# Optimization experiments

Measured on AMD Instinct MI355X. Metric: run time of the kernel, lower is better.

## Reference

```python
import jax, jax.numpy as jnp
import numpy as np

B, L, D_MODEL = 2, 2048, 1024
D_INNER, D_STATE, D_CONV, DT_RANK = 2048, 16, 4, 64  # expand=2, dt_rank=ceil(1024/16)


def setup_inputs() -> dict:
    key = jax.random.key(0)
    ks = jax.random.split(key, 12)
    s = lambda k, shape, sc=0.02: jax.random.normal(k, shape, dtype=jnp.float32) * sc
    return {
        "x": jax.random.normal(ks[0], (B, L, D_MODEL), dtype=jnp.float32),
        "norm_w": jnp.ones((D_MODEL,), jnp.float32),
        "norm_b": jnp.zeros((D_MODEL,), jnp.float32),
        "in_proj_w": s(ks[1], (2 * D_INNER, D_MODEL)),
        "conv_w": s(ks[2], (D_INNER, 1, D_CONV), 0.1),
        "conv_b": s(ks[3], (D_INNER,), 0.1),
        "x_proj_w": s(ks[4], (DT_RANK + 2 * D_STATE, D_INNER)),
        "dt_proj_w": s(ks[5], (D_INNER, DT_RANK), 0.1),
        "dt_proj_b": s(ks[6], (D_INNER,), 0.5),
        "A_log": jnp.log(jnp.broadcast_to(jnp.arange(1, D_STATE + 1, dtype=jnp.float32), (D_INNER, D_STATE))),
        "D": jnp.ones((D_INNER,), jnp.float32),
        "out_proj_w": s(ks[7], (D_MODEL, D_INNER)),
    }


def _layernorm(x, w, b, eps=1e-5):
    mu = jnp.mean(x, axis=-1, keepdims=True)
    var = jnp.var(x, axis=-1, keepdims=True)
    return (x - mu) * jax.lax.rsqrt(var + eps) * w + b


def _mamba_forward(x, norm_w, norm_b, in_proj_w, conv_w, conv_b, x_proj_w,
                   dt_proj_w, dt_proj_b, A_log, D, out_proj_w):
    residual = x
    xn = _layernorm(x, norm_w, norm_b)
    # in_proj -> split into x-branch and gate z
    xz = jnp.einsum('bld,ed->ble', xn, in_proj_w)  # [B,L,2*D_INNER]
    xc, z = jnp.split(xz, 2, axis=-1)
    # causal depthwise conv1d over time
    xt = jnp.transpose(xc, (0, 2, 1))  # [B,C,L]
    xt = jnp.pad(xt, ((0, 0), (0, 0), (D_CONV - 1, 0)))
    xt = jax.lax.conv_general_dilated(
        xt, conv_w, window_strides=(1,), padding=[(0, 0)],
        feature_group_count=D_INNER,
        dimension_numbers=('NCH', 'OIH', 'NCH')) + conv_b[None, :, None]
    u = jax.nn.silu(jnp.transpose(xt, (0, 2, 1)))  # [B,L,D_INNER]
    # input-dependent dt, B, C
    x_dbl = jnp.einsum('bld,ed->ble', u, x_proj_w)
    dt, Bm, Cm = jnp.split(x_dbl, [DT_RANK, DT_RANK + D_STATE], axis=-1)
    dt = jax.nn.softplus(jnp.einsum('blr,dr->bld', dt, dt_proj_w) + dt_proj_b)  # [B,L,D_INNER]
    A = -jnp.exp(A_log)  # [D_INNER, D_STATE]

    def step(h, inp):
        dt_t, B_t, C_t, u_t = inp  # [B,Di],[B,Ds],[B,Ds],[B,Di]
        dA = jnp.exp(dt_t[..., None] * A)                       # [B,Di,Ds]
        h = dA * h + (dt_t * u_t)[..., None] * B_t[:, None, :]  # [B,Di,Ds]
        y_t = jnp.einsum('bds,bs->bd', h, C_t)
        return h, y_t

    xs = (jnp.transpose(dt, (1, 0, 2)), jnp.transpose(Bm, (1, 0, 2)),
          jnp.transpose(Cm, (1, 0, 2)), jnp.transpose(u, (1, 0, 2)))
    h0 = jnp.zeros((B, D_INNER, D_STATE), dtype=x.dtype)
    _, ys = jax.lax.scan(step, h0, xs)
    y = jnp.transpose(ys, (1, 0, 2)) + u * D  # [B,L,D_INNER]
    y = y * jax.nn.silu(z)
    out = jnp.einsum('ble,de->bld', y, out_proj_w)
    # dropout in eval mode = identity
    return residual + out


def reference(x, norm_w, norm_b, in_proj_w, conv_w, conv_b, x_proj_w,
              dt_proj_w, dt_proj_b, A_log, D, out_proj_w):
    return _mamba_forward(x, norm_w, norm_b, in_proj_w, conv_w, conv_b, x_proj_w,
                          dt_proj_w, dt_proj_b, A_log, D, out_proj_w)
```

## Files before the change

kernel.cpp:

```cpp
#include <hip/hip_runtime.h>
#include <hip/hip_bf16.h>
#include <math.h>

#define BB 2
#define LL 2048
#define DMODEL 1024
#define DINNER 2048
#define DSTATE 16
#define DTRANK 64
#define NROWS (BB * LL)
#define NC 32
#define CK 64

typedef __bf16 bf16x8 __attribute__((ext_vector_type(8)));
typedef float  f32x4  __attribute__((ext_vector_type(4)));
typedef __attribute__((address_space(3))) void       as3_void;
typedef const __attribute__((address_space(1))) void as1_cvoid;

__device__ __forceinline__ ushort f2bf(float x) {
    __hip_bfloat16 h = __float2bfloat16(x);
    return *(ushort*)&h;
}

__global__ __launch_bounds__(256) void ln_kernel(const float* __restrict__ x,
                                                 const float* __restrict__ w,
                                                 const float* __restrict__ b,
                                                 __hip_bfloat16* __restrict__ xn) {
    int row = blockIdx.x;
    const float* xr = x + (size_t)row * DMODEL;
    float4 v = reinterpret_cast<const float4*>(xr)[threadIdx.x];
    float s  = v.x + v.y + v.z + v.w;
    float ss = v.x * v.x + v.y * v.y + v.z * v.z + v.w * v.w;
    for (int off = 32; off > 0; off >>= 1) {
        s  += __shfl_down(s, off);
        ss += __shfl_down(ss, off);
    }
    __shared__ float red0[4], red1[4];
    __shared__ float mu_s, rstd_s;
    int lane = threadIdx.x & 63, wv = threadIdx.x >> 6;
    if (lane == 0) { red0[wv] = s; red1[wv] = ss; }
    __syncthreads();
    if (threadIdx.x == 0) {
        float S = red0[0] + red0[1] + red0[2] + red0[3];
        float SS = red1[0] + red1[1] + red1[2] + red1[3];
        float mu = S * (1.0f / DMODEL);
        float var = SS * (1.0f / DMODEL) - mu * mu;
        mu_s = mu;
        rstd_s = rsqrtf(var + 1e-5f);
    }
    __syncthreads();
    float mu = mu_s, rstd = rstd_s;
    float4 wv4 = reinterpret_cast<const float4*>(w)[threadIdx.x];
    float4 bv4 = reinterpret_cast<const float4*>(b)[threadIdx.x];
    ushort4 o;
    o.x = f2bf((v.x - mu) * rstd * wv4.x + bv4.x);
    o.y = f2bf((v.y - mu) * rstd * wv4.y + bv4.y);
    o.z = f2bf((v.z - mu) * rstd * wv4.z + bv4.z);
    o.w = f2bf((v.w - mu) * rstd * wv4.w + bv4.w);
    *reinterpret_cast<ushort4*>((ushort*)xn + (size_t)row * DMODEL + threadIdx.x * 4) = o;
}

__global__ __launch_bounds__(256) void cvt_kernel(const float* __restrict__ in,
                                                  __hip_bfloat16* __restrict__ o) {
    int i = (blockIdx.x * 256 + threadIdx.x) * 4;
    float4 v = *reinterpret_cast<const float4*>(in + i);
    ushort4 p;
    p.x = f2bf(v.x); p.y = f2bf(v.y); p.z = f2bf(v.z); p.w = f2bf(v.w);
    *reinterpret_cast<ushort4*>((ushort*)o + i) = p;
}

template <int EPI>
__global__ __launch_bounds__(256) void gemm_bf16(
    const __hip_bfloat16* __restrict__ A, int lda,
    const __hip_bfloat16* __restrict__ W, int ldw,
    float* __restrict__ C, float* __restrict__ C2, int nsplit, int ldc,
    int K, const float* __restrict__ R) {
    __shared__ ushort As[128][32];
    __shared__ ushort Bs[128][32];
    int tid = threadIdx.x;
    int w = tid >> 6, lane = tid & 63;
    int m0 = blockIdx.y * 128, n0 = blockIdx.x * 128;
    int wr = w >> 1, wc = w & 1;

    int srow = (w << 4) + (lane >> 2);
    int skoff = (lane & 3) << 3;
    const ushort* gA = (const ushort*)A + (size_t)(m0 + srow) * lda + skoff;
    const ushort* gB = (const ushort*)W + (size_t)(n0 + srow) * ldw + skoff;
    char* ldsA0 = (char*)&As[0][0] + w * 1024;
    char* ldsB0 = (char*)&Bs[0][0] + w * 1024;

    f32x4 acc[4][4] = {};
    int frow = (lane & 15);
    int fk   = (lane >> 4) << 3;

    for (int k0 = 0; k0 < K; k0 += 32) {
        __syncthreads();
        __builtin_amdgcn_global_load_lds((as1_cvoid*)(gA + k0),                 (as3_void*)(ldsA0),        16, 0, 0);
        __builtin_amdgcn_global_load_lds((as1_cvoid*)(gA + (size_t)64 * lda + k0), (as3_void*)(ldsA0 + 4096), 16, 0, 0);
        __builtin_amdgcn_global_load_lds((as1_cvoid*)(gB + k0),                 (as3_void*)(ldsB0),        16, 0, 0);
        __builtin_amdgcn_global_load_lds((as1_cvoid*)(gB + (size_t)64 * ldw + k0), (as3_void*)(ldsB0 + 4096), 16, 0, 0);
        __syncthreads();

        bf16x8 af[4], bfr[4];
#pragma unroll
        for (int mi = 0; mi < 4; mi++)
            af[mi] = *(const bf16x8*)&As[wr * 64 + mi * 16 + frow][fk];
#pragma unroll
        for (int ni = 0; ni < 4; ni++)
            bfr[ni] = *(const bf16x8*)&Bs[wc * 64 + ni * 16 + frow][fk];
#pragma unroll
        for (int mi = 0; mi < 4; mi++)
#pragma unroll
            for (int ni = 0; ni < 4; ni++)
                acc[mi][ni] = __builtin_amdgcn_mfma_f32_16x16x32_bf16(
                    af[mi], bfr[ni], acc[mi][ni], 0, 0, 0);
    }

    int crow = (lane >> 4) << 2;
    int ccol = lane & 15;
    float* Cb = C;
    int nbase = n0;
    if (EPI == 0 && n0 >= nsplit) { Cb = C2; nbase = n0 - nsplit; }
#pragma unroll
    for (int mi = 0; mi < 4; mi++) {
#pragma unroll
        for (int ni = 0; ni < 4; ni++) {
#pragma unroll
            for (int r = 0; r < 4; r++) {
                int m = m0 + wr * 64 + mi * 16 + crow + r;
                int n = nbase + wc * 64 + ni * 16 + ccol;
                float v = acc[mi][ni][r];
                if (EPI == 2) v += R[(size_t)m * ldc + n];
                Cb[(size_t)m * ldc + n] = v;
            }
        }
    }
}

template <int EPI>
__global__ __launch_bounds__(256) void gemm_kernel(
    const float* __restrict__ A, int lda,
    const float* __restrict__ W, int ldw,
    float* __restrict__ C, int ldc,
    int N, int K,
    const float* __restrict__ bias) {
    __shared__ float As[16][64];
    __shared__ float Ws[16][64];
    int m0 = blockIdx.y * 64;
    int n0 = blockIdx.x * 64;
    int tid = threadIdx.x;
    int tm = tid >> 4, tn = tid & 15;
    int lr = tid >> 2;
    int lk = (tid & 3) << 2;

    float acc[4][4] = {};

    for (int k0 = 0; k0 < K; k0 += 16) {
        float4 av = *reinterpret_cast<const float4*>(A + (size_t)(m0 + lr) * lda + k0 + lk);
        float4 wvv;
        int wn = n0 + lr;
        if (wn < N)
            wvv = *reinterpret_cast<const float4*>(W + (size_t)wn * ldw + k0 + lk);
        else
            wvv = make_float4(0.f, 0.f, 0.f, 0.f);
        __syncthreads();
        As[lk + 0][lr] = av.x; As[lk + 1][lr] = av.y;
        As[lk + 2][lr] = av.z; As[lk + 3][lr] = av.w;
        Ws[lk + 0][lr] = wvv.x; Ws[lk + 1][lr] = wvv.y;
        Ws[lk + 2][lr] = wvv.z; Ws[lk + 3][lr] = wvv.w;
        __syncthreads();
#pragma unroll
        for (int k = 0; k < 16; k++) {
            float4 a = *reinterpret_cast<const float4*>(&As[k][tm << 2]);
            float4 bv = *reinterpret_cast<const float4*>(&Ws[k][tn << 2]);
            float ar[4] = {a.x, a.y, a.z, a.w};
            float br[4] = {bv.x, bv.y, bv.z, bv.w};
#pragma unroll
            for (int i = 0; i < 4; i++)
#pragma unroll
                for (int j = 0; j < 4; j++)
                    acc[i][j] = fmaf(ar[i], br[j], acc[i][j]);
        }
    }
#pragma unroll
    for (int i = 0; i < 4; i++) {
        int m = m0 + (tm << 2) + i;
#pragma unroll
        for (int j = 0; j < 4; j++) {
            int n = n0 + (tn << 2) + j;
            if (n < N) {
                float v = acc[i][j];
                if (EPI == 1) {
                    v += bias[n];
                    v = (v > 20.f) ? v : log1pf(__expf(v));
                }
                C[(size_t)m * ldc + n] = v;
            }
        }
    }
}

__global__ __launch_bounds__(256) void conv_silu_kernel(
    const float* __restrict__ xc, const float* __restrict__ cw,
    const float* __restrict__ cb, float* __restrict__ u) {
    int c = blockIdx.x * 256 + threadIdx.x;
    int r = blockIdx.y;
    int l = r & (LL - 1);
    float4 wv = reinterpret_cast<const float4*>(cw)[c];
    const float* p = xc + (size_t)r * DINNER + c;
    float acc = cb[c];
    if (l >= 3) acc = fmaf(p[-3 * DINNER], wv.x, acc);
    if (l >= 2) acc = fmaf(p[-2 * DINNER], wv.y, acc);
    if (l >= 1) acc = fmaf(p[-1 * DINNER], wv.z, acc);
    acc = fmaf(p[0], wv.w, acc);
    float sig = 1.f / (1.f + __expf(-acc));
    u[(size_t)r * DINNER + c] = acc * sig;
}

__global__ __launch_bounds__(256) void scan_pass1(
    const float* __restrict__ dt, const float* __restrict__ u,
    const float* __restrict__ xdbl, const float* __restrict__ A_log,
    float* __restrict__ hloc, float* __restrict__ aprod) {
    int bc = blockIdx.x >> 3;
    int b = bc >> 5, c = bc & (NC - 1);
    int d = ((blockIdx.x & 7) << 8) + threadIdx.x;
    float a2[DSTATE];
#pragma unroll
    for (int s = 0; s < DSTATE; s++)
        a2[s] = -__expf(A_log[d * DSTATE + s]) * 1.44269504089f;
    float h[DSTATE], ap[DSTATE];
#pragma unroll
    for (int s = 0; s < DSTATE; s++) { h[s] = 0.f; ap[s] = 1.f; }

    int t0 = c * CK;
    const float* dtp = dt + ((size_t)b * LL + t0) * DINNER + d;
    const float* up  = u  + ((size_t)b * LL + t0) * DINNER + d;
    const float* xr0 = xdbl + ((size_t)b * LL + t0) * 96;

    for (int t = 0; t < CK; t++) {
        float dtv = dtp[(size_t)t * DINNER];
        float uv  = up[(size_t)t * DINNER];
        float du  = dtv * uv;
        const float* xr = xr0 + t * 96;
#pragma unroll
        for (int s = 0; s < DSTATE; s++) {
            float dA = exp2f(dtv * a2[s]);
            h[s] = fmaf(dA, h[s], du * xr[64 + s]);
            ap[s] *= dA;
        }
    }
    size_t base = ((size_t)bc * DSTATE) * DINNER + d;
#pragma unroll
    for (int s = 0; s < DSTATE; s++) {
        hloc[base + (size_t)s * DINNER]  = h[s];
        aprod[base + (size_t)s * DINNER] = ap[s];
    }
}

__global__ __launch_bounds__(256) void scan_pass2(
    float* __restrict__ hloc, const float* __restrict__ aprod) {
    int idx = blockIdx.x * 256 + threadIdx.x;
    int d = idx & (DINNER - 1);
    int s = (idx >> 11) & (DSTATE - 1);
    int b = idx >> 15;
    float run = 0.f;
    for (int c = 0; c < NC; c++) {
        size_t off = ((size_t)((b * NC + c) * DSTATE + s)) * DINNER + d;
        float hl = hloc[off];
        float ap = aprod[off];
        hloc[off] = run;
        run = fmaf(ap, run, hl);
    }
}

__global__ __launch_bounds__(256) void scan_pass3(
    const float* __restrict__ dt, const float* __restrict__ u,
    const float* __restrict__ xdbl, const float* __restrict__ zb,
    const float* __restrict__ A_log, const float* __restrict__ Dp,
    const float* __restrict__ hinit, __hip_bfloat16* __restrict__ y) {
    int bc = blockIdx.x >> 3;
    int b = bc >> 5, c = bc & (NC - 1);
    int d = ((blockIdx.x & 7) << 8) + threadIdx.x;
    float a2[DSTATE];
#pragma unroll
    for (int s = 0; s < DSTATE; s++)
        a2[s] = -__expf(A_log[d * DSTATE + s]) * 1.44269504089f;
    float Dd = Dp[d];
    float h[DSTATE];
    size_t base = ((size_t)bc * DSTATE) * DINNER + d;
#pragma unroll
    for (int s = 0; s < DSTATE; s++) h[s] = hinit[base + (size_t)s * DINNER];

    int t0 = c * CK;
    const float* dtp = dt + ((size_t)b * LL + t0) * DINNER + d;
    const float* up  = u  + ((size_t)b * LL + t0) * DINNER + d;
    const float* zp  = zb + ((size_t)b * LL + t0) * DINNER + d;
    const float* xr0 = xdbl + ((size_t)b * LL + t0) * 96;
    ushort* yp = (ushort*)y + ((size_t)b * LL + t0) * DINNER + d;

    for (int t = 0; t < CK; t++) {
        float dtv = dtp[(size_t)t * DINNER];
        float uv  = up[(size_t)t * DINNER];
        float du  = dtv * uv;
        const float* xr = xr0 + t * 96;
        float yv = 0.f;
#pragma unroll
        for (int s = 0; s < DSTATE; s++) {
            float dA = exp2f(dtv * a2[s]);
            h[s] = fmaf(dA, h[s], du * xr[64 + s]);
            yv = fmaf(h[s], xr[80 + s], yv);
        }
        float zv = zp[(size_t)t * DINNER];
        float sig = 1.f / (1.f + __expf(-zv));
        yv = (yv + uv * Dd) * (zv * sig);
        yp[(size_t)t * DINNER] = f2bf(yv);
    }
}

extern "C" void kernel_launch(void* const* d_in, const int* in_sizes, int n_in,
                              void* d_out, int out_size, void* d_ws, size_t ws_size,
                              hipStream_t stream) {
    const float* x         = (const float*)d_in[0];
    const float* norm_w    = (const float*)d_in[1];
    const float* norm_b    = (const float*)d_in[2];
    const float* in_proj_w = (const float*)d_in[3];
    const float* conv_w    = (const float*)d_in[4];
    const float* conv_b    = (const float*)d_in[5];
    const float* x_proj_w  = (const float*)d_in[6];
    const float* dt_proj_w = (const float*)d_in[7];
    const float* dt_proj_b = (const float*)d_in[8];
    const float* A_log     = (const float*)d_in[9];
    const float* Dp        = (const float*)d_in[10];
    const float* out_proj_w= (const float*)d_in[11];
    float* out = (float*)d_out;

    float* ws   = (float*)d_ws;
    const size_t NI = (size_t)NROWS * DINNER;
    float* xc   = ws;
    float* zb   = xc + NI;
    float* u    = zb + NI;
    float* dtb  = u + NI;
    float* xdbl = dtb + NI;
    __hip_bfloat16* xnb = (__hip_bfloat16*)(xdbl + (size_t)NROWS * 96);
    __hip_bfloat16* ybb = xnb + (size_t)NROWS * DMODEL;
    __hip_bfloat16* wib = ybb + NI;
    __hip_bfloat16* wob = wib + (size_t)2 * DINNER * DMODEL;
    float* hloc  = xc;
    float* aprod = xc + (size_t)BB * NC * DSTATE * DINNER;

    ln_kernel<<<NROWS, 256, 0, stream>>>(x, norm_w, norm_b, xnb);
    cvt_kernel<<<(2 * DINNER * DMODEL) / 1024, 256, 0, stream>>>(in_proj_w, wib);
    cvt_kernel<<<(DMODEL * DINNER) / 1024, 256, 0, stream>>>(out_proj_w, wob);
    gemm_bf16<0><<<dim3((2 * DINNER) / 128, NROWS / 128), 256, 0, stream>>>(
        xnb, DMODEL, wib, DMODEL, xc, zb, DINNER, DINNER, DMODEL, nullptr);
    conv_silu_kernel<<<dim3(DINNER / 256, NROWS), 256, 0, stream>>>(xc, conv_w, conv_b, u);
    gemm_kernel<0><<<dim3(2, NROWS / 64), 256, 0, stream>>>(
        u, DINNER, x_proj_w, DINNER, xdbl, 96, 96, DINNER, nullptr);
    gemm_kernel<1><<<dim3(DINNER / 64, NROWS / 64), 256, 0, stream>>>(
        xdbl, 96, dt_proj_w, DTRANK, dtb, DINNER, DINNER, DTRANK, dt_proj_b);
    scan_pass1<<<BB * NC * (DINNER / 256), 256, 0, stream>>>(dtb, u, xdbl, A_log, hloc, aprod);
    scan_pass2<<<(BB * DSTATE * DINNER) / 256, 256, 0, stream>>>(hloc, aprod);
    scan_pass3<<<BB * NC * (DINNER / 256), 256, 0, stream>>>(dtb, u, xdbl, zb, A_log, Dp, hloc, ybb);
    gemm_bf16<2><<<dim3(DMODEL / 128, NROWS / 128), 256, 0, stream>>>(
        ybb, DINNER, wob, DINNER, out, nullptr, 1 << 30, DMODEL, DINNER, x);
}
```

Measured before the change: 487.6 us.

## Split-K the x_proj GEMM into partial sums plus a reduction kernel

Replaces the x_proj GEMM, which launched only 128 blocks over a K of 2048, with a split-K version that cuts K into 16 chunks (2048 blocks). A second kernel then sums the partial results. The goal is to fill the GPU's compute units on this narrow-N GEMM, at the cost of writing and re-reading 16 partial 4096x96 buffers (stored in the dt buffer before it is used) and one extra launch.

```diff
diff --git a/kernel.cpp b/kernel.cpp
--- a/kernel.cpp
+++ b/kernel.cpp
@@ -11,6 +11,8 @@
 #define NROWS (BB * LL)
 #define NC 32
 #define CK 64
+#define KS 16
+#define KCH (DINNER / KS)
 
 typedef __bf16 bf16x8 __attribute__((ext_vector_type(8)));
 typedef float  f32x4  __attribute__((ext_vector_type(4)));
@@ -95,9 +97,9 @@
 
     for (int k0 = 0; k0 < K; k0 += 32) {
         __syncthreads();
-        __builtin_amdgcn_global_load_lds((as1_cvoid*)(gA + k0),                 (as3_void*)(ldsA0),        16, 0, 0);
+        __builtin_amdgcn_global_load_lds((as1_cvoid*)(gA + k0),                    (as3_void*)(ldsA0),        16, 0, 0);
         __builtin_amdgcn_global_load_lds((as1_cvoid*)(gA + (size_t)64 * lda + k0), (as3_void*)(ldsA0 + 4096), 16, 0, 0);
-        __builtin_amdgcn_global_load_lds((as1_cvoid*)(gB + k0),                 (as3_void*)(ldsB0),        16, 0, 0);
+        __builtin_amdgcn_global_load_lds((as1_cvoid*)(gB + k0),                    (as3_void*)(ldsB0),        16, 0, 0);
         __builtin_amdgcn_global_load_lds((as1_cvoid*)(gB + (size_t)64 * ldw + k0), (as3_void*)(ldsB0 + 4096), 16, 0, 0);
         __syncthreads();
 
@@ -198,6 +200,72 @@
             }
         }
     }
+}
+
+__global__ __launch_bounds__(256) void xp_partial(
+    const float* __restrict__ A,
+    const float* __restrict__ W,
+    float* __restrict__ P) {
+    __shared__ float As[16][64];
+    __shared__ float Ws[16][64];
+    int m0 = blockIdx.y * 64;
+    int n0 = blockIdx.x * 64;
+    int kbase = blockIdx.z * KCH;
+    int tid = threadIdx.x;
+    int tm = tid >> 4, tn = tid & 15;
+    int lr = tid >> 2;
+    int lk = (tid & 3) << 2;
+
+    float acc[4][4] = {};
+
+    for (int k0 = kbase; k0 < kbase + KCH; k0 += 16) {
+        float4 av = *reinterpret_cast<const float4*>(A + (size_t)(m0 + lr) * DINNER + k0 + lk);
+        float4 wvv;
+        int wn = n0 + lr;
+        if (wn < 96)
+            wvv = *reinterpret_cast<const float4*>(W + (size_t)wn * DINNER + k0 + lk);
+        else
+            wvv = make_float4(0.f, 0.f, 0.f, 0.f);
+        __syncthreads();
+        As[lk + 0][lr] = av.x; As[lk + 1][lr] = av.y;
+        As[lk + 2][lr] = av.z; As[lk + 3][lr] = av.w;
+        Ws[lk + 0][lr] = wvv.x; Ws[lk + 1][lr] = wvv.y;
+        Ws[lk + 2][lr] = wvv.z; Ws[lk + 3][lr] = wvv.w;
+        __syncthreads();
+#pragma unroll
+        for (int k = 0; k < 16; k++) {
+            float4 a = *reinterpret_cast<const float4*>(&As[k][tm << 2]);
+            float4 bv = *reinterpret_cast<const float4*>(&Ws[k][tn << 2]);
+            float ar[4] = {a.x, a.y, a.z, a.w};
+            float br[4] = {bv.x, bv.y, bv.z, bv.w};
+#pragma unroll
+            for (int i = 0; i < 4; i++)
+#pragma unroll
+                for (int j = 0; j < 4; j++)
+                    acc[i][j] = fmaf(ar[i], br[j], acc[i][j]);
+        }
+    }
+    float* Pz = P + (size_t)blockIdx.z * NROWS * 96;
+#pragma unroll
+    for (int i = 0; i < 4; i++) {
+        int m = m0 + (tm << 2) + i;
+#pragma unroll
+        for (int j = 0; j < 4; j++) {
+            int n = n0 + (tn << 2) + j;
+            if (n < 96)
+                Pz[(size_t)m * 96 + n] = acc[i][j];
+        }
+    }
+}
+
+__global__ __launch_bounds__(256) void xp_reduce(
+    const float* __restrict__ P, float* __restrict__ xdbl) {
+    int i = blockIdx.x * 256 + threadIdx.x;
+    float s = 0.f;
+#pragma unroll
+    for (int z = 0; z < KS; z++)
+        s += P[(size_t)z * NROWS * 96 + i];
+    xdbl[i] = s;
 }
 
 __global__ __launch_bounds__(256) void conv_silu_kernel(
@@ -347,6 +415,7 @@
     __hip_bfloat16* wob = wib + (size_t)2 * DINNER * DMODEL;
     float* hloc  = xc;
     float* aprod = xc + (size_t)BB * NC * DSTATE * DINNER;
+    float* xpp   = dtb;
 
     ln_kernel<<<NROWS, 256, 0, stream>>>(x, norm_w, norm_b, xnb);
     cvt_kernel<<<(2 * DINNER * DMODEL) / 1024, 256, 0, stream>>>(in_proj_w, wib);
@@ -354,8 +423,8 @@
     gemm_bf16<0><<<dim3((2 * DINNER) / 128, NROWS / 128), 256, 0, stream>>>(
         xnb, DMODEL, wib, DMODEL, xc, zb, DINNER, DINNER, DMODEL, nullptr);
     conv_silu_kernel<<<dim3(DINNER / 256, NROWS), 256, 0, stream>>>(xc, conv_w, conv_b, u);
-    gemm_kernel<0><<<dim3(2, NROWS / 64), 256, 0, stream>>>(
-        u, DINNER, x_proj_w, DINNER, xdbl, 96, 96, DINNER, nullptr);
+    xp_partial<<<dim3(2, NROWS / 64, KS), 256, 0, stream>>>(u, x_proj_w, xpp);
+    xp_reduce<<<(NROWS * 96) / 256, 256, 0, stream>>>(xpp, xdbl);
     gemm_kernel<1><<<dim3(DINNER / 64, NROWS / 64), 256, 0, stream>>>(
         xdbl, 96, dt_proj_w, DTRANK, dtb, DINNER, DINNER, DTRANK, dt_proj_b);
     scan_pass1<<<BB * NC * (DINNER / 256), 256, 0, stream>>>(dtb, u, xdbl, A_log, hloc, aprod);
```

Result: faster. 430.4 us (-11.7%).
